# Kernel tuning notes

Measured on AMD Instinct MI355X. Metric: run time of the kernel, lower is better.

The kernel has to match this reference:

```python
import jax, jax.numpy as jnp
import numpy as np

N_NODES = 100000
N_EDGES = 1600000
D_IN = 64
D_OUT = 64
BN_EPS = 1e-5


def setup_inputs() -> dict:
    key = jax.random.key(0)
    k_x, k_src, k_dst, k_ew, k_w = jax.random.split(key, 5)
    x = jax.random.normal(k_x, (N_NODES, D_IN), dtype=jnp.float32)
    edge_src = jax.random.randint(k_src, (N_EDGES,), 0, N_NODES, dtype=jnp.int32)
    edge_dst = jax.random.randint(k_dst, (N_EDGES,), 0, N_NODES, dtype=jnp.int32)
    edge_weight = jax.random.uniform(k_ew, (N_EDGES,), dtype=jnp.float32)
    # Xavier-uniform weight, zero bias (reset_parameters)
    limit = float(np.sqrt(6.0 / (D_IN + D_OUT)))
    W = jax.random.uniform(k_w, (D_IN, D_OUT), dtype=jnp.float32, minval=-limit, maxval=limit)
    bias = jnp.zeros((D_OUT,), dtype=jnp.float32)
    gamma = jnp.ones((D_OUT,), dtype=jnp.float32)
    beta = jnp.zeros((D_OUT,), dtype=jnp.float32)
    return {"x": x, "edge_src": edge_src, "edge_dst": edge_dst,
            "edge_weight": edge_weight, "W": W, "bias": bias,
            "gamma": gamma, "beta": beta}


def reference(x, edge_src, edge_dst, edge_weight, W, bias, gamma, beta):
    # GraphConvolution: support = x @ W  -> [N, D_OUT]
    support = jnp.matmul(x, W)
    # spmm(adj, support) with adj in COO form: out[d] += w_e * support[s]
    msgs = edge_weight[:, None] * support[edge_src]        # [E, D_OUT]
    agg = jax.ops.segment_sum(msgs, edge_dst, num_segments=N_NODES)
    out = agg + bias
    # BatchNorm1d (training mode: batch statistics over node dim)
    mean = jnp.mean(out, axis=0)
    var = jnp.var(out, axis=0)
    out = (out - mean) * jax.lax.rsqrt(var + BN_EPS) * gamma + beta
    # ReLU activation; dropout is identity in deterministic/inference mode
    return jax.nn.relu(out)
```

## Files before the change

### kernel.cpp

```cpp
#include <hip/hip_runtime.h>
#include <hip/hip_bf16.h>

#define NN 100000
#define NE 1600000
#define DD 64
#define NCOARSE 392
#define GEMM_TILES 1563
#define PLACE_EPB 2048
#define PLACE_BLOCKS 784
#define LCNT_STRIDE 788
#define EMAX 6016

__device__ inline unsigned short f2bf(float f) {
    __hip_bfloat16 h = __float2bfloat16(f);
    unsigned short s; __builtin_memcpy(&s, &h, 2); return s;
}

__global__ __launch_bounds__(256) void k_hist(const int* __restrict__ edst,
                                              int* __restrict__ lcntT) {
    __shared__ int h[NCOARSE];
    for (int i = threadIdx.x; i < NCOARSE; i += 256) h[i] = 0;
    __syncthreads();
    const int e0 = blockIdx.x * PLACE_EPB;
#pragma unroll
    for (int k = 0; k < 8; ++k) {
        int e = e0 + k * 256 + threadIdx.x;
        if (e < NE) atomicAdd(&h[edst[e] >> 8], 1);
    }
    __syncthreads();
    for (int i = threadIdx.x; i < NCOARSE; i += 256)
        lcntT[i * LCNT_STRIDE + blockIdx.x] = h[i];
}

__global__ __launch_bounds__(1024) void k_colscan(int* __restrict__ lcntT,
                                                  int* __restrict__ cnt) {
    int* col = lcntT + blockIdx.x * LCNT_STRIDE;
    const int t = threadIdx.x;
    const int v = (t < PLACE_BLOCKS) ? col[t] : 0;
    __shared__ int sc[1024];
    sc[t] = v; __syncthreads();
    for (int o = 1; o < 1024; o <<= 1) {
        int u = (t >= o) ? sc[t - o] : 0;
        __syncthreads();
        sc[t] += u;
        __syncthreads();
    }
    if (t < PLACE_BLOCKS) col[t] = sc[t] - v;
    if (t == 1023) cnt[blockIdx.x] = sc[1023];
}

__global__ __launch_bounds__(512) void k_scan392(const int* __restrict__ cnt,
                                                 int* __restrict__ cstart) {
    __shared__ int sc[512];
    const int t = threadIdx.x;
    const int v = (t < NCOARSE) ? cnt[t] : 0;
    sc[t] = v; __syncthreads();
    for (int o = 1; o < 512; o <<= 1) {
        int u = (t >= o) ? sc[t - o] : 0;
        __syncthreads();
        sc[t] += u;
        __syncthreads();
    }
    if (t < NCOARSE) cstart[t] = sc[t] - v;
    if (t == 0) cstart[NCOARSE] = NE;
}

__global__ __launch_bounds__(256) void k_gemm_scatter(const float* __restrict__ x,
                                                      const float* __restrict__ Wg,
                                                      unsigned* __restrict__ support2,
                                                      const int* __restrict__ esrc,
                                                      const int* __restrict__ edst,
                                                      const float* __restrict__ ew,
                                                      const int* __restrict__ cstart,
                                                      const int* __restrict__ lcntT,
                                                      int2* __restrict__ permA) {
    if (blockIdx.x < PLACE_BLOCKS) {
        const int blk = blockIdx.x;
        __shared__ int loff[NCOARSE];
        for (int i = threadIdx.x; i < NCOARSE; i += 256)
            loff[i] = cstart[i] + lcntT[i * LCNT_STRIDE + blk];
        __syncthreads();
        const int e0 = blk * PLACE_EPB;
#pragma unroll
        for (int k = 0; k < 8; ++k) {
            int e = e0 + k * 256 + threadIdx.x;
            if (e < NE) {
                int d = edst[e];
                int p = atomicAdd(&loff[d >> 8], 1);
                permA[p] = make_int2(esrc[e] | ((d & 255) << 17), __float_as_int(ew[e]));
            }
        }
        return;
    }

    __shared__ float Xs[64 * DD];
    const int r0 = (blockIdx.x - PLACE_BLOCKS) * 64;
    const int nrows = (r0 + 64 <= NN) ? 64 : (NN - r0);
    const int t = threadIdx.x;

    const float4* xg = (const float4*)(x + (size_t)r0 * DD);
    for (int i = t; i < nrows * 16; i += 256) {
        const int row = i >> 4, k4 = i & 15;
        *(float4*)&Xs[row * 64 + ((k4 ^ (row & 15)) << 2)] = xg[i];
    }
    if (nrows < 64) {
        for (int i = nrows * 16 + t; i < 64 * 16; i += 256)
            ((float4*)Xs)[i] = make_float4(0.f, 0.f, 0.f, 0.f);
    }
    __syncthreads();

    const int lane = t & 63;
    const int w = __builtin_amdgcn_readfirstlane(t >> 6);
    const float* Wp = Wg + w * 16;

    float acc[16];
#pragma unroll
    for (int c = 0; c < 16; ++c) acc[c] = 0.f;

#pragma unroll 4
    for (int k4 = 0; k4 < 16; ++k4) {
        const float4 xv = *(const float4*)&Xs[lane * 64 + ((k4 ^ (lane & 15)) << 2)];
        const float* wr = Wp + k4 * 4 * DD;
#pragma unroll
        for (int c = 0; c < 16; ++c) {
            acc[c] = fmaf(xv.x, wr[c],          acc[c]);
            acc[c] = fmaf(xv.y, wr[DD + c],     acc[c]);
            acc[c] = fmaf(xv.z, wr[2 * DD + c], acc[c]);
            acc[c] = fmaf(xv.w, wr[3 * DD + c], acc[c]);
        }
    }

    __syncthreads();
    unsigned* Us = (unsigned*)Xs;
#pragma unroll
    for (int j = 0; j < 8; ++j) {
        const unsigned p = (unsigned)f2bf(acc[2 * j]) |
                           ((unsigned)f2bf(acc[2 * j + 1]) << 16);
        const int cp = 8 * w + j;
        Us[lane * 32 + ((cp + lane) & 31)] = p;
    }
    __syncthreads();
    uint4* sg = (uint4*)(support2 + (size_t)r0 * 32);
#pragma unroll
    for (int it = 0; it < 2; ++it) {
        const int g4 = t + it * 256;
        const int row = g4 >> 3, c0 = (g4 & 7) << 2;
        if (row < nrows) {
            uint4 v;
            v.x = Us[row * 32 + ((c0 + 0 + row) & 31)];
            v.y = Us[row * 32 + ((c0 + 1 + row) & 31)];
            v.z = Us[row * 32 + ((c0 + 2 + row) & 31)];
            v.w = Us[row * 32 + ((c0 + 3 + row) & 31)];
            sg[g4] = v;
        }
    }
}

__global__ __launch_bounds__(1024, 8) void k_sortgather(const int* __restrict__ cstart,
                                                        const int2* __restrict__ permA,
                                                        const uint4* __restrict__ support4,
                                                        float* __restrict__ out,
                                                        float* __restrict__ pstat) {
    __shared__ int2 eL[EMAX];
    __shared__ unsigned short idx16[EMAX];
    __shared__ int cnt[256], st[257], cur[256], wtot[4];
    __shared__ float red[16][128];

    const int c = blockIdx.x, t = threadIdx.x;
    const int cs = cstart[c];
    const int sz = min(cstart[c + 1] - cs, EMAX);
    const int wave = t >> 6, lane = t & 63;

    for (int j = t; j < sz; j += 1024) eL[j] = permA[cs + j];
    if (t < 256) cnt[t] = 0;
    __syncthreads();

    for (int j = t; j < sz; j += 1024)
        atomicAdd(&cnt[(eL[j].x >> 17) & 255], 1);
    __syncthreads();

    int v = 0, xv = 0;
    if (wave < 4) {
        v = cnt[t]; xv = v;
#pragma unroll
        for (int o = 1; o < 64; o <<= 1) {
            int u = __shfl_up(xv, o, 64);
            if (lane >= o) xv += u;
        }
        if (lane == 63) wtot[wave] = xv;
    }
    __syncthreads();
    if (t < 4) {
        int w0 = wtot[t], xw = w0;
#pragma unroll
        for (int o = 1; o < 4; o <<= 1) {
            int u = __shfl_up(xw, o, 64);
            if (t >= o) xw += u;
        }
        wtot[t] = xw - w0;
    }
    __syncthreads();
    if (wave < 4) {
        const int base = wtot[wave] + xv - v;
        st[t] = base;
        cur[t] = base;
    }
    if (t == 0) st[256] = sz;
    __syncthreads();

    for (int j = t; j < sz; j += 1024) {
        int p = atomicAdd(&cur[(eL[j].x >> 17) & 255], 1);
        idx16[p] = (unsigned short)j;
    }
    __syncthreads();

    const int sub = lane >> 3, q = lane & 7;
    const int node0 = c * 256;
    float sacc[8] = {0.f, 0.f, 0.f, 0.f, 0.f, 0.f, 0.f, 0.f};
    float sqacc[8] = {0.f, 0.f, 0.f, 0.f, 0.f, 0.f, 0.f, 0.f};
    for (int n = wave; n < 256; n += 16) {
        const int bs = st[n], be = st[n + 1];
        float acc[8] = {0.f, 0.f, 0.f, 0.f, 0.f, 0.f, 0.f, 0.f};
        for (int j0 = bs; j0 < be; j0 += 8) {
            const int j = j0 + sub;
            if (j < be) {
                const int2 m = eL[idx16[j]];
                const uint4 p = support4[(size_t)(m.x & 0x1FFFF) * 8 + q];
                const float w = __int_as_float(m.y);
                acc[0] = fmaf(w, __uint_as_float(p.x << 16), acc[0]);
                acc[1] = fmaf(w, __uint_as_float(p.x & 0xffff0000u), acc[1]);
                acc[2] = fmaf(w, __uint_as_float(p.y << 16), acc[2]);
                acc[3] = fmaf(w, __uint_as_float(p.y & 0xffff0000u), acc[3]);
                acc[4] = fmaf(w, __uint_as_float(p.z << 16), acc[4]);
                acc[5] = fmaf(w, __uint_as_float(p.z & 0xffff0000u), acc[5]);
                acc[6] = fmaf(w, __uint_as_float(p.w << 16), acc[6]);
                acc[7] = fmaf(w, __uint_as_float(p.w & 0xffff0000u), acc[7]);
            }
        }
#pragma unroll
        for (int i = 0; i < 8; ++i) {
            acc[i] += __shfl_xor(acc[i], 8, 64);
            acc[i] += __shfl_xor(acc[i], 16, 64);
            acc[i] += __shfl_xor(acc[i], 32, 64);
        }
        const int node = node0 + n;
        if (sub == 0 && node < NN) {
            float* op = out + (size_t)node * DD + q * 8;
            *(float4*)op = make_float4(acc[0], acc[1], acc[2], acc[3]);
            *(float4*)(op + 4) = make_float4(acc[4], acc[5], acc[6], acc[7]);
#pragma unroll
            for (int k = 0; k < 8; ++k) {
                sacc[k] += acc[k];
                sqacc[k] = fmaf(acc[k], acc[k], sqacc[k]);
            }
        }
    }

    if (sub == 0) {
#pragma unroll
        for (int k = 0; k < 8; ++k) {
            red[wave][q * 8 + k] = sacc[k];
            red[wave][64 + q * 8 + k] = sqacc[k];
        }
    }
    __syncthreads();
    if (t < 128) {
        float a = 0.f;
#pragma unroll
        for (int wv = 0; wv < 16; ++wv) a += red[wv][t];
        pstat[c * 128 + t] = a;
    }
}

__global__ __launch_bounds__(128) void k_finstats(const float* __restrict__ pstat,
                                                  float* __restrict__ ss,
                                                  const float* __restrict__ gamma,
                                                  const float* __restrict__ beta) {
    const int t = threadIdx.x;
    float acc = 0.f;
    for (int b = 0; b < NCOARSE; ++b)
        acc += pstat[b * 128 + t];
    __shared__ float red[2 * DD];
    red[t] = acc;
    __syncthreads();
    if (t < DD) {
        const float invn = 1.0f / NN;
        float mean = red[t] * invn;
        float var = fmaxf(red[DD + t] * invn - mean * mean, 0.f);
        float sc = rsqrtf(var + 1e-5f) * gamma[t];
        ss[t] = sc;
        ss[DD + t] = beta[t] - mean * sc;
    }
}

__global__ __launch_bounds__(256) void k_final(float* __restrict__ out,
                                               const float* __restrict__ ss) {
    const size_t idx = ((size_t)blockIdx.x * 256 + threadIdx.x) * 4;
    const int c = (int)(idx & 63);
    float4 v = *(const float4*)(out + idx);
    float4 o;
    o.x = fmaxf(fmaf(v.x, ss[c + 0], ss[DD + c + 0]), 0.f);
    o.y = fmaxf(fmaf(v.y, ss[c + 1], ss[DD + c + 1]), 0.f);
    o.z = fmaxf(fmaf(v.z, ss[c + 2], ss[DD + c + 2]), 0.f);
    o.w = fmaxf(fmaf(v.w, ss[c + 3], ss[DD + c + 3]), 0.f);
    *(float4*)(out + idx) = o;
}

extern "C" void kernel_launch(void* const* d_in, const int* in_sizes, int n_in,
                              void* d_out, int out_size, void* d_ws, size_t ws_size,
                              hipStream_t stream) {
    const float* x     = (const float*)d_in[0];
    const int*   esrc  = (const int*)d_in[1];
    const int*   edst  = (const int*)d_in[2];
    const float* ew    = (const float*)d_in[3];
    const float* W     = (const float*)d_in[4];
    const float* gamma = (const float*)d_in[6];
    const float* beta  = (const float*)d_in[7];
    float*       out   = (float*)d_out;

    char* ws = (char*)d_ws;
    unsigned* support2 = (unsigned*)ws;  ws += (size_t)NN * DD * 2;
    int2*     permA  = (int2*)ws;     ws += (size_t)NE * 8;
    int*   lcntT  = (int*)ws;    ws += NCOARSE * LCNT_STRIDE * 4;
    int*   cnt    = (int*)ws;    ws += NCOARSE * 4;
    float* ss     = (float*)ws;  ws += 128 * 4;
    int*   cstart = (int*)ws;    ws += (NCOARSE + 4) * 4;
    float* pstat  = (float*)ws;  ws += (size_t)NCOARSE * 128 * 4;

    k_hist        <<<PLACE_BLOCKS, 256, 0, stream>>>(edst, lcntT);
    k_colscan     <<<NCOARSE, 1024, 0, stream>>>(lcntT, cnt);
    k_scan392     <<<1, 512, 0, stream>>>(cnt, cstart);
    k_gemm_scatter<<<PLACE_BLOCKS + GEMM_TILES, 256, 0, stream>>>(
                      x, W, support2, esrc, edst, ew, cstart, lcntT, permA);
    k_sortgather  <<<NCOARSE, 1024, 0, stream>>>(cstart, permA,
                      (const uint4*)support2, out, pstat);
    k_finstats    <<<1, 128, 0, stream>>>(pstat, ss, gamma, beta);
    k_final       <<<NN * DD / 4 / 256, 256, 0, stream>>>(out, ss);
}
```

Baseline: 204.8 us.

## Replace histogram-scan edge binning with fixed-capacity buckets and global atomic counters

```diff
diff --git a/kernel.cpp b/kernel.cpp
--- a/kernel.cpp
+++ b/kernel.cpp
@@ -8,61 +8,15 @@
 #define GEMM_TILES 1563
 #define PLACE_EPB 2048
 #define PLACE_BLOCKS 784
-#define LCNT_STRIDE 788
-#define EMAX 6016
+#define CAP 4736
 
 __device__ inline unsigned short f2bf(float f) {
     __hip_bfloat16 h = __float2bfloat16(f);
     unsigned short s; __builtin_memcpy(&s, &h, 2); return s;
 }
 
-__global__ __launch_bounds__(256) void k_hist(const int* __restrict__ edst,
-                                              int* __restrict__ lcntT) {
-    __shared__ int h[NCOARSE];
-    for (int i = threadIdx.x; i < NCOARSE; i += 256) h[i] = 0;
-    __syncthreads();
-    const int e0 = blockIdx.x * PLACE_EPB;
-#pragma unroll
-    for (int k = 0; k < 8; ++k) {
-        int e = e0 + k * 256 + threadIdx.x;
-        if (e < NE) atomicAdd(&h[edst[e] >> 8], 1);
-    }
-    __syncthreads();
-    for (int i = threadIdx.x; i < NCOARSE; i += 256)
-        lcntT[i * LCNT_STRIDE + blockIdx.x] = h[i];
-}
-
-__global__ __launch_bounds__(1024) void k_colscan(int* __restrict__ lcntT,
-                                                  int* __restrict__ cnt) {
-    int* col = lcntT + blockIdx.x * LCNT_STRIDE;
-    const int t = threadIdx.x;
-    const int v = (t < PLACE_BLOCKS) ? col[t] : 0;
-    __shared__ int sc[1024];
-    sc[t] = v; __syncthreads();
-    for (int o = 1; o < 1024; o <<= 1) {
-        int u = (t >= o) ? sc[t - o] : 0;
-        __syncthreads();
-        sc[t] += u;
-        __syncthreads();
-    }
-    if (t < PLACE_BLOCKS) col[t] = sc[t] - v;
-    if (t == 1023) cnt[blockIdx.x] = sc[1023];
-}
-
-__global__ __launch_bounds__(512) void k_scan392(const int* __restrict__ cnt,
-                                                 int* __restrict__ cstart) {
-    __shared__ int sc[512];
-    const int t = threadIdx.x;
-    const int v = (t < NCOARSE) ? cnt[t] : 0;
-    sc[t] = v; __syncthreads();
-    for (int o = 1; o < 512; o <<= 1) {
-        int u = (t >= o) ? sc[t - o] : 0;
-        __syncthreads();
-        sc[t] += u;
-        __syncthreads();
-    }
-    if (t < NCOARSE) cstart[t] = sc[t] - v;
-    if (t == 0) cstart[NCOARSE] = NE;
+__global__ __launch_bounds__(512) void k_zero(int* __restrict__ gcnt) {
+    if (threadIdx.x < NCOARSE) gcnt[threadIdx.x] = 0;
 }
 
 __global__ __launch_bounds__(256) void k_gemm_scatter(const float* __restrict__ x,
@@ -71,23 +25,37 @@
                                                       const int* __restrict__ esrc,
                                                       const int* __restrict__ edst,
                                                       const float* __restrict__ ew,
-                                                      const int* __restrict__ cstart,
-                                                      const int* __restrict__ lcntT,
+                                                      int* __restrict__ gcnt,
                                                       int2* __restrict__ permA) {
     if (blockIdx.x < PLACE_BLOCKS) {
         const int blk = blockIdx.x;
+        __shared__ int h[NCOARSE];
         __shared__ int loff[NCOARSE];
-        for (int i = threadIdx.x; i < NCOARSE; i += 256)
-            loff[i] = cstart[i] + lcntT[i * LCNT_STRIDE + blk];
+        for (int i = threadIdx.x; i < NCOARSE; i += 256) h[i] = 0;
         __syncthreads();
         const int e0 = blk * PLACE_EPB;
+        int dreg[8];
 #pragma unroll
         for (int k = 0; k < 8; ++k) {
-            int e = e0 + k * 256 + threadIdx.x;
-            if (e < NE) {
-                int d = edst[e];
-                int p = atomicAdd(&loff[d >> 8], 1);
-                permA[p] = make_int2(esrc[e] | ((d & 255) << 17), __float_as_int(ew[e]));
+            const int e = e0 + k * 256 + threadIdx.x;
+            dreg[k] = (e < NE) ? edst[e] : -1;
+            if (dreg[k] >= 0) atomicAdd(&h[dreg[k] >> 8], 1);
+        }
+        __syncthreads();
+        for (int i = threadIdx.x; i < NCOARSE; i += 256) {
+            const int hc = h[i];
+            loff[i] = i * CAP + ((hc > 0) ? atomicAdd(&gcnt[i], hc) : 0);
+        }
+        __syncthreads();
+#pragma unroll
+        for (int k = 0; k < 8; ++k) {
+            if (dreg[k] >= 0) {
+                const int e = e0 + k * 256 + threadIdx.x;
+                const int d = dreg[k];
+                const int c = d >> 8;
+                const int p = atomicAdd(&loff[c], 1);
+                if (p < c * CAP + CAP)
+                    permA[p] = make_int2(esrc[e] | ((d & 255) << 17), __float_as_int(ew[e]));
             }
         }
         return;
@@ -156,19 +124,19 @@
     }
 }
 
-__global__ __launch_bounds__(1024, 8) void k_sortgather(const int* __restrict__ cstart,
+__global__ __launch_bounds__(1024, 8) void k_sortgather(const int* __restrict__ gcnt,
                                                         const int2* __restrict__ permA,
                                                         const uint4* __restrict__ support4,
                                                         float* __restrict__ out,
                                                         float* __restrict__ pstat) {
-    __shared__ int2 eL[EMAX];
-    __shared__ unsigned short idx16[EMAX];
+    __shared__ int2 eL[CAP];
+    __shared__ unsigned short idx16[CAP];
     __shared__ int cnt[256], st[257], cur[256], wtot[4];
     __shared__ float red[16][128];
 
     const int c = blockIdx.x, t = threadIdx.x;
-    const int cs = cstart[c];
-    const int sz = min(cstart[c + 1] - cs, EMAX);
+    const int cs = c * CAP;
+    const int sz = min(gcnt[c], CAP);
     const int wave = t >> 6, lane = t & 63;
 
     for (int j = t; j < sz; j += 1024) eL[j] = permA[cs + j];
@@ -320,19 +288,15 @@
 
     char* ws = (char*)d_ws;
     unsigned* support2 = (unsigned*)ws;  ws += (size_t)NN * DD * 2;
-    int2*     permA  = (int2*)ws;     ws += (size_t)NE * 8;
-    int*   lcntT  = (int*)ws;    ws += NCOARSE * LCNT_STRIDE * 4;
-    int*   cnt    = (int*)ws;    ws += NCOARSE * 4;
+    int2*     permA  = (int2*)ws;     ws += (size_t)NCOARSE * CAP * 8;
+    int*   gcnt   = (int*)ws;    ws += NCOARSE * 4;
     float* ss     = (float*)ws;  ws += 128 * 4;
-    int*   cstart = (int*)ws;    ws += (NCOARSE + 4) * 4;
     float* pstat  = (float*)ws;  ws += (size_t)NCOARSE * 128 * 4;
 
-    k_hist        <<<PLACE_BLOCKS, 256, 0, stream>>>(edst, lcntT);
-    k_colscan     <<<NCOARSE, 1024, 0, stream>>>(lcntT, cnt);
-    k_scan392     <<<1, 512, 0, stream>>>(cnt, cstart);
+    k_zero        <<<1, 512, 0, stream>>>(gcnt);
     k_gemm_scatter<<<PLACE_BLOCKS + GEMM_TILES, 256, 0, stream>>>(
-                      x, W, support2, esrc, edst, ew, cstart, lcntT, permA);
-    k_sortgather  <<<NCOARSE, 1024, 0, stream>>>(cstart, permA,
+                      x, W, support2, esrc, edst, ew, gcnt, permA);
+    k_sortgather  <<<NCOARSE, 1024, 0, stream>>>(gcnt, permA,
                       (const uint4*)support2, out, pstat);
     k_finstats    <<<1, 128, 0, stream>>>(pstat, ss, gamma, beta);
     k_final       <<<NN * DD / 4 / 256, 256, 0, stream>>>(out, ss);
```

Measured after the change: 203.6 us. About the same (-0.6%).
